# Performance work log

Measured on AMD Instinct MI355X. Metric: run time of the kernel, lower is better.

The kernel has to match this reference:

```python
import jax, jax.numpy as jnp
import numpy as np

IMG_DIM = 28 * 28


def _distmat(X):
    # D[i,j] = ||x_i||^2 - 2 x_i.x_j + ||x_j||^2
    r = jnp.sum(X * X, axis=1)
    a = X @ X.T
    return r[:, None] - 2.0 * a + r[None, :]


def _sigma_from_self(D, m):
    """Replicates sigma_estimation(X, X): median of the strict lower triangle of
    distmat(cat([X, X])), which is the 2x2 block-tiled matrix [[D,D],[D,D]].
    Its strict lower triangle multiset = full D (block 2,1) + 2x strict tril(D).
    Clamps: if med<=0 use mean; floor at 0.01. Detached (stop_gradient), matching
    the torch .detach().cpu().numpy() path."""
    mask = jnp.tril(jnp.ones((m, m), dtype=bool), -1)
    tril_inf = jnp.where(mask, D, jnp.inf)
    vals = jnp.concatenate([D.ravel(), tril_inf.ravel(), tril_inf.ravel()])
    s = jnp.sort(vals)  # inf padding sorts to the end
    k = 2 * m * m - m  # number of strict-lower-triangle entries of a 2m x 2m matrix
    if k % 2 == 0:
        med = 0.5 * (s[k // 2 - 1] + s[k // 2])  # np.median averages middles
    else:
        med = s[(k - 1) // 2]
    tri_sum = jnp.sum(jnp.where(mask, D, 0.0))
    mean_tri = (jnp.sum(D) + 2.0 * tri_sum) / k
    med = jnp.where(med <= 0.0, mean_tri, med)
    med = jnp.maximum(med, 0.01)
    return jax.lax.stop_gradient(med)


def _centered_kernel(D, sigma):
    # Kxc = Kx @ (I - ones/m)  ==  Kx - rowmean(Kx)
    K = jnp.exp(-D / (2.0 * sigma * sigma))
    return K - jnp.mean(K, axis=1, keepdims=True)


def _hsic_norm_from_kernels(Kxc, Kyc):
    Pxy = jnp.mean(Kxc * Kyc.T)
    Px = jnp.sqrt(jnp.mean(Kxc * Kxc.T))
    Py = jnp.sqrt(jnp.mean(Kyc * Kyc.T))
    return Pxy / (Px * Py)


def reference(x, y):
    x2 = x.reshape((-1, IMG_DIM))  # [m, 784]
    m = x2.shape[0]
    d = y.shape[-1]

    # hsic_normalized(x, y) with per-variable median sigma
    Dx = _distmat(x2)
    Dy = _distmat(y)
    Kx = _centered_kernel(Dx, _sigma_from_self(Dx, m))
    Ky = _centered_kernel(Dy, _sigma_from_self(Dy, m))
    mi_io = _hsic_norm_from_kernels(Kx, Ky)

    # Batched version of the nested loop over latent component pairs (i<j).
    # Per-column 1-D distance matrices: [d, m, m]
    yt = y.T  # [d, m]
    Dc = (yt[:, :, None] - yt[:, None, :]) ** 2
    sig = jax.vmap(lambda D: _sigma_from_self(D, m))(Dc)  # [d]
    Kc = jnp.exp(-Dc / (2.0 * sig * sig)[:, None, None])
    Kc = Kc - jnp.mean(Kc, axis=2, keepdims=True)  # centered, [d, m, m]

    # P[a,b] = mean(K_a * K_b^T)
    P = jnp.einsum('aij,bji->ab', Kc, Kc) / (m * m)
    diag = jnp.diagonal(P)
    norm = P / jnp.sqrt(diag[:, None] * diag[None, :])
    pair_mask = jnp.triu(jnp.ones((d, d), dtype=bool), 1)  # i < j
    mi_component_sum = jnp.sum(jnp.where(pair_mask, norm, 0.0))

    return -mi_io + mi_component_sum


def setup_inputs() -> dict:
    key = jax.random.key(0)
    kx, ky = jax.random.split(key)
    x = jax.random.normal(kx, (2048, 784), dtype=jnp.float32)
    y = jax.random.normal(ky, (2048, 10), dtype=jnp.float32)
    return {"x": x, "y": y}
```

## Files before the change

### kernel.cpp

```cpp
#include <hip/hip_runtime.h>
#include <math.h>

constexpr int Md   = 2048;
constexpr int NDIM = 784;
constexpr int DYC  = 10;
constexpr int MM   = Md * Md;
constexpr unsigned RANK_LO = 4193279u;
constexpr unsigned RANK_HI = 4193280u;
constexpr int NPROB = 12;
constexpr int NB    = 256;
constexpr int NBINS = 8192;
constexpr int NTRI  = 528;

constexpr size_t OFF_DX     = 0;
constexpr size_t OFF_DY     = OFF_DX + (size_t)MM * 4;
constexpr size_t OFF_RX     = OFF_DY + (size_t)MM * 4;
constexpr size_t OFF_RY     = OFF_RX + Md * 8;
constexpr size_t OFF_RC     = OFF_RY + Md * 8;
constexpr size_t OFF_GACC   = OFF_RC + (size_t)DYC * Md * 8;
constexpr size_t OFF_HISTA  = OFF_GACC + 64 * 8;
constexpr size_t OFF_HISTB  = OFF_HISTA + (size_t)NPROB * NBINS * 4;
constexpr size_t OFF_RES    = OFF_HISTB + (size_t)NPROB * NBINS * 4;
constexpr size_t OFF_JOBS   = OFF_RES + 72 * 8;
constexpr size_t OFF_Q      = OFF_JOBS + NPROB * 5 * 4;
constexpr size_t OFF_RXN    = OFF_Q + NPROB * 4;
constexpr size_t OFF_YT     = OFF_RXN + Md * 4;
constexpr size_t WS_NEED    = OFF_YT + (size_t)DYC * Md * 4;
constexpr size_t ZERO_BASE  = OFF_GACC;
constexpr size_t ZERO_LEN   = OFF_JOBS - OFF_GACC;

typedef _Float16 f16x8 __attribute__((ext_vector_type(8)));
typedef _Float16 f16x4 __attribute__((ext_vector_type(4)));
typedef float    f32x16 __attribute__((ext_vector_type(16)));

__device__ __forceinline__ unsigned fkey(float v) {
  unsigned u = __float_as_uint(v);
  return (u & 0x80000000u) ? ~u : (u | 0x80000000u);
}
__device__ __forceinline__ float keyinv(unsigned k) {
  unsigned u = (k & 0x80000000u) ? (k ^ 0x80000000u) : ~k;
  return __uint_as_float(u);
}
__device__ __forceinline__ f16x8 ld8(const _Float16* p) {
  f16x4 lo = *(const f16x4*)p;
  f16x4 hi = *(const f16x4*)(p + 4);
  f16x8 r;
  r[0]=lo[0]; r[1]=lo[1]; r[2]=lo[2]; r[3]=lo[3];
  r[4]=hi[0]; r[5]=hi[1]; r[6]=hi[2]; r[7]=hi[3];
  return r;
}
__device__ __forceinline__ double waveReduceD(double v) {
  #pragma unroll
  for (int o = 32; o > 0; o >>= 1) v += __shfl_down(v, o, 64);
  return v;
}
__device__ __forceinline__ double blockReduceD(double v) {
  __shared__ double sred[4];
  v = waveReduceD(v);
  int lane = threadIdx.x & 63;
  int w    = threadIdx.x >> 6;
  __syncthreads();
  if (lane == 0) sred[w] = v;
  __syncthreads();
  double r = 0.0;
  if (threadIdx.x == 0) { r = sred[0] + sred[1] + sred[2] + sred[3]; }
  return r;
}

__global__ void fail_kernel(float* out) { if (threadIdx.x == 0) out[0] = 0.0f; }

__global__ __launch_bounds__(256) void prep_kernel(const float* __restrict__ X,
                                                   const float* __restrict__ Y,
                                                   float* __restrict__ rxn,
                                                   float* __restrict__ Yt,
                                                   unsigned* __restrict__ jobs) {
  int bb = blockIdx.x;
  if (bb < Md) {
    double acc = 0.0;
    for (int k = threadIdx.x; k < NDIM; k += 256) {
      float v = X[bb * NDIM + k];
      acc += (double)v * (double)v;
    }
    double r = blockReduceD(acc);
    if (threadIdx.x == 0) rxn[bb] = (float)r;
  } else if (bb < Md + 80) {
    int e = (bb - Md) * 256 + threadIdx.x;
    if (e < Md * DYC) {
      int i = e / DYC, c = e % DYC;
      Yt[c * Md + i] = Y[e];
    }
  } else {
    int t = threadIdx.x;
    if (t < NPROB * 5) {
      int w = t % 5;
      jobs[t] = (w == 1) ? RANK_LO : (w == 3) ? RANK_HI : 0u;
    }
  }
}

__global__ __launch_bounds__(256) void dist_kernel(const float* __restrict__ X,
                                                   const float* __restrict__ Y,
                                                   const float* __restrict__ rxn,
                                                   float* __restrict__ Dx,
                                                   float* __restrict__ Dy) {
  __shared__ _Float16 Ah[64][68], Al[64][68], Bh[64][68], Bl[64][68];
  __shared__ float Yi[64][10], Yj[64][10];
  const int tid = threadIdx.x;
  int t0 = blockIdx.x;
  int bi = (int)((sqrtf(8.0f * (float)t0 + 1.0f) - 1.0f) * 0.5f);
  while ((bi + 1) * (bi + 2) / 2 <= t0) ++bi;
  while (bi * (bi + 1) / 2 > t0) --bi;
  int bj = t0 - bi * (bi + 1) / 2;
  const int i0 = bi * 64, j0 = bj * 64;
  const bool offdiag = (bi != bj);

  if (blockIdx.z == 1) {
    for (int t = tid; t < 640; t += 256) {
      int r = t / 10, c = t % 10;
      Yi[r][c] = Y[(i0 + r) * DYC + c];
      Yj[r][c] = Y[(j0 + r) * DYC + c];
    }
    __syncthreads();
    int jj = tid & 63;
    int ii0 = (tid >> 6) * 16;
    float yj[10];
    #pragma unroll
    for (int c = 0; c < 10; ++c) yj[c] = Yj[jj][c];
    for (int r = 0; r < 16; ++r) {
      int ii = ii0 + r;
      float s = 0.f;
      #pragma unroll
      for (int c = 0; c < 10; ++c) { float d = Yi[ii][c] - yj[c]; s = fmaf(d, d, s); }
      Dy[(size_t)(i0 + ii) * Md + (j0 + jj)] = s;
      if (offdiag) Dy[(size_t)(j0 + jj) * Md + (i0 + ii)] = s;
    }
    return;
  }

  const int wave = tid >> 6, lane = tid & 63;
  const int wr = (wave >> 1) * 32, wc = (wave & 1) * 32;
  const int srow = tid >> 2;
  const int sseg = (tid & 3) * 8;

  f32x16 acc_hh = {}, acc_c1 = {}, acc_c2 = {};

  const float* Arow = X + (size_t)(i0 + srow) * NDIM;
  const float* Brow = X + (size_t)(j0 + srow) * NDIM;
  const int lrow = lane & 31;
  const int lko  = (lane >> 5) * 8;

  for (int k0 = 0; k0 < 800; k0 += 32) {
    float a[8], b[8];
    if (k0 + 32 <= NDIM) {
      float4 a4 = *(const float4*)(Arow + k0 + sseg);
      float4 a5 = *(const float4*)(Arow + k0 + sseg + 4);
      float4 b4 = *(const float4*)(Brow + k0 + sseg);
      float4 b5 = *(const float4*)(Brow + k0 + sseg + 4);
      a[0]=a4.x; a[1]=a4.y; a[2]=a4.z; a[3]=a4.w; a[4]=a5.x; a[5]=a5.y; a[6]=a5.z; a[7]=a5.w;
      b[0]=b4.x; b[1]=b4.y; b[2]=b4.z; b[3]=b4.w; b[4]=b5.x; b[5]=b5.y; b[6]=b5.z; b[7]=b5.w;
    } else {
      #pragma unroll
      for (int u = 0; u < 8; ++u) {
        int k = k0 + sseg + u;
        a[u] = (k < NDIM) ? Arow[k] : 0.0f;
        b[u] = (k < NDIM) ? Brow[k] : 0.0f;
      }
    }
    __syncthreads();
    #pragma unroll
    for (int half = 0; half < 2; ++half) {
      f16x4 vah, val_, vbh, vbl;
      #pragma unroll
      for (int u = 0; u < 4; ++u) {
        float av = a[half * 4 + u];
        _Float16 h = (_Float16)av;
        vah[u] = h; val_[u] = (_Float16)(av - (float)h);
        float bv = b[half * 4 + u];
        _Float16 g = (_Float16)bv;
        vbh[u] = g; vbl[u] = (_Float16)(bv - (float)g);
      }
      *(f16x4*)&Ah[srow][sseg + half * 4] = vah;
      *(f16x4*)&Al[srow][sseg + half * 4] = val_;
      *(f16x4*)&Bh[srow][sseg + half * 4] = vbh;
      *(f16x4*)&Bl[srow][sseg + half * 4] = vbl;
    }
    __syncthreads();
    #pragma unroll
    for (int ks = 0; ks < 2; ++ks) {
      int ko = ks * 16 + lko;
      f16x8 fah = ld8(&Ah[wr + lrow][ko]);
      f16x8 fal = ld8(&Al[wr + lrow][ko]);
      f16x8 fbh = ld8(&Bh[wc + lrow][ko]);
      f16x8 fbl = ld8(&Bl[wc + lrow][ko]);
      acc_hh = __builtin_amdgcn_mfma_f32_32x32x16_f16(fah, fbh, acc_hh, 0, 0, 0);
      acc_c1 = __builtin_amdgcn_mfma_f32_32x32x16_f16(fah, fbl, acc_c1, 0, 0, 0);
      acc_c2 = __builtin_amdgcn_mfma_f32_32x32x16_f16(fal, fbh, acc_c2, 0, 0, 0);
    }
  }
  int col = j0 + wc + (lane & 31);
  float rj = rxn[col];
  #pragma unroll
  for (int r = 0; r < 16; ++r) {
    int row = i0 + wr + (r & 3) + 8 * (r >> 2) + 4 * (lane >> 5);
    float t = rxn[row] + rj;
    float cc = acc_c1[r] + acc_c2[r];
    float v = fmaf(-2.0f, cc, fmaf(-2.0f, acc_hh[r], t));
    Dx[(size_t)row * Md + col] = v;
    if (offdiag) Dx[(size_t)col * Md + row] = v;
  }
}

__global__ __launch_bounds__(256) void hist_kernel(const float* __restrict__ Dx,
                                                   const float* __restrict__ Dy,
                                                   const float* __restrict__ Yt,
                                                   unsigned* __restrict__ histA,
                                                   unsigned* __restrict__ histB,
                                                   const unsigned* __restrict__ jobs,
                                                   int level) {
  __shared__ unsigned lh[NBINS];
  __shared__ float ycol[Md];
  int prob = blockIdx.y;
  for (int b = threadIdx.x; b < NBINS; b += 256) lh[b] = 0;
  const float* Mptr = (prob == 0) ? Dx : (prob == 1 ? Dy : nullptr);
  if (prob >= 2) {
    const float* src = Yt + (size_t)(prob - 2) * Md;
    for (int i = threadIdx.x; i < Md; i += 256) ycol[i] = src[i];
  }
  __syncthreads();
  unsigned pfxL = jobs[prob * 5 + 0];
  unsigned pfxH = jobs[prob * 5 + 2];
  unsigned div  = jobs[prob * 5 + 4];
  unsigned* ghB = histB + prob * NBINS;

  auto histo = [&](float v, unsigned w) {
    unsigned key = fkey(v);
    if (level == 0) {
      atomicAdd(&lh[key >> 19], w);
    } else if (level == 1) {
      if ((key >> 19) == pfxL)             atomicAdd(&lh[(key >> 6) & 8191u], w);
      else if (div && (key >> 19) == pfxH) atomicAdd(&ghB[(key >> 6) & 8191u], w);
    } else {
      if ((key >> 6) == pfxL)              atomicAdd(&lh[key & 63u], w);
      else if (div && (key >> 6) == pfxH)  atomicAdd(&ghB[key & 63u], w);
    }
  };

  for (int r = 0; r < Md / NB; ++r) {
    int i = blockIdx.x + r * NB;
    int n = i + 1, ng = n >> 2, tail = n & 3;
    if (Mptr) {
      const float4* row4 = (const float4*)(Mptr + (size_t)i * Md);
      for (int g = threadIdx.x; g < ng; g += 256) {
        float4 v = row4[g];
        int jb = g << 2;
        histo(v.x, (jb == i) ? 1u : 4u);
        histo(v.y, (jb + 1 == i) ? 1u : 4u);
        histo(v.z, (jb + 2 == i) ? 1u : 4u);
        histo(v.w, (jb + 3 == i) ? 1u : 4u);
      }
      if (threadIdx.x < tail) {
        int j = (ng << 2) + threadIdx.x;
        histo(Mptr[(size_t)i * Md + j], (j == i) ? 1u : 4u);
      }
    } else {
      float yi = ycol[i];
      for (int g = threadIdx.x; g < ng; g += 256) {
        float4 y4 = *(const float4*)&ycol[g << 2];
        int jb = g << 2;
        float d0 = yi - y4.x, d1 = yi - y4.y, d2 = yi - y4.z, d3 = yi - y4.w;
        histo(d0 * d0, (jb == i) ? 1u : 4u);
        histo(d1 * d1, (jb + 1 == i) ? 1u : 4u);
        histo(d2 * d2, (jb + 2 == i) ? 1u : 4u);
        histo(d3 * d3, (jb + 3 == i) ? 1u : 4u);
      }
      if (threadIdx.x < tail) {
        int j = (ng << 2) + threadIdx.x;
        float d = yi - ycol[j];
        histo(d * d, (j == i) ? 1u : 4u);
      }
    }
  }
  __syncthreads();
  unsigned* ghA = histA + prob * NBINS;
  for (int b = threadIdx.x; b < NBINS; b += 256) {
    unsigned v = lh[b];
    if (v) atomicAdd(&ghA[b], v);
  }
}

__global__ __launch_bounds__(256) void select_kernel(unsigned* __restrict__ histA,
                                                     unsigned* __restrict__ histB,
                                                     unsigned* __restrict__ jobs,
                                                     float* __restrict__ q,
                                                     int level) {
  __shared__ unsigned lhA[NBINS], lhB[NBINS];
  __shared__ unsigned psA[256], psB[256];
  int prob = blockIdx.x;
  int nbins = (level == 2) ? 64 : NBINS;
  int C = (nbins + 255) / 256;
  unsigned* ghA = histA + prob * NBINS;
  unsigned* ghB = histB + prob * NBINS;
  unsigned sA = 0, sB = 0;
  for (int k = 0; k < C; ++k) {
    int b = threadIdx.x * C + k;
    if (b < nbins) {
      unsigned v = ghA[b]; lhA[b] = v; sA += v;
      unsigned u = ghB[b]; lhB[b] = u; sB += u;
    }
  }
  psA[threadIdx.x] = sA; psB[threadIdx.x] = sB;
  __syncthreads();
  if (threadIdx.x == 0) {
    unsigned pfxL = jobs[prob * 5 + 0], remL = jobs[prob * 5 + 1];
    unsigned pfxH = jobs[prob * 5 + 2], remH = jobs[prob * 5 + 3];
    unsigned wasdiv = jobs[prob * 5 + 4];

    auto scan = [&](const unsigned* ps, const unsigned* lhp, unsigned r,
                    int& bin, unsigned& cum) {
      unsigned c = 0; int t = 0;
      for (; t < 255; ++t) { if (c + ps[t] > r) break; c += ps[t]; }
      int b = t * C;
      int be = b + C - 1; if (be > nbins - 1) be = nbins - 1;
      for (; b < be; ++b) { if (c + lhp[b] > r) break; c += lhp[b]; }
      bin = b; cum = c;
    };

    int bL; unsigned cL; scan(psA, lhA, remL, bL, cL);
    int bH; unsigned cH;
    unsigned div = wasdiv;
    if (!wasdiv) {
      scan(psA, lhA, remH, bH, cH);
      if (bH != bL) div = 1;
    } else {
      scan(psB, lhB, remH, bH, cH);
    }
    unsigned baseH = wasdiv ? pfxH : pfxL;
    if (level < 2) {
      jobs[prob * 5 + 0] = (level == 0) ? (unsigned)bL : ((pfxL << 13) | (unsigned)bL);
      jobs[prob * 5 + 2] = (level == 0) ? (unsigned)bH : ((baseH << 13) | (unsigned)bH);
      jobs[prob * 5 + 1] = remL - cL;
      jobs[prob * 5 + 3] = remH - cH;
      jobs[prob * 5 + 4] = div;
    } else {
      unsigned keyL = (pfxL << 6) | (unsigned)bL;
      unsigned keyH = (baseH << 6) | (unsigned)bH;
      float med = 0.5f * (keyinv(keyL) + keyinv(keyH));
      med = fmaxf(med, 0.01f);
      q[prob] = 2.0f * med * med;
    }
  }
  __syncthreads();
  for (int b = threadIdx.x; b < nbins; b += 256) { ghA[b] = 0; ghB[b] = 0; }
}

__global__ __launch_bounds__(256) void phase3a_kernel(const float* __restrict__ Dx,
                                                      const float* __restrict__ Dy,
                                                      const float* __restrict__ Yt,
                                                      const float* __restrict__ q,
                                                      double* __restrict__ Rx,
                                                      double* __restrict__ Ry,
                                                      double* __restrict__ Rc,
                                                      double* __restrict__ gacc) {
  __shared__ double shred[12];
  const int wave = threadIdx.x >> 6, lane = threadIdx.x & 63;
  int bb = blockIdx.x;

  if (bb < 256) {
    const float qx = q[0], qy = q[1];
    double gxx = 0, gxy = 0, gyy = 0;
    #pragma unroll
    for (int rr = 0; rr < 2; ++rr) {
      int i = bb * 4 + wave + rr * 1024;
      const float4* rx4 = (const float4*)(Dx + (size_t)i * Md);
      const float4* ry4 = (const float4*)(Dy + (size_t)i * Md);
      double ax = 0, ay = 0;
      #pragma unroll
      for (int it = 0; it < 8; ++it) {
        float4 xv = rx4[it * 64 + lane];
        float4 yv = ry4[it * 64 + lane];
        #pragma unroll
        for (int u = 0; u < 4; ++u) {
          float xe = (u == 0) ? xv.x : (u == 1) ? xv.y : (u == 2) ? xv.z : xv.w;
          float ye = (u == 0) ? yv.x : (u == 1) ? yv.y : (u == 2) ? yv.z : yv.w;
          float ex = expm1f(-(xe / qx));
          float ey = expm1f(-(ye / qy));
          ax += (double)ex; ay += (double)ey;
          gxx += (double)ex * ex;
          gxy += (double)ex * ey;
          gyy += (double)ey * ey;
        }
      }
      ax = waveReduceD(ax);
      ay = waveReduceD(ay);
      if (lane == 0) { Rx[i] = ax; Ry[i] = ay; }
    }
    gxx = waveReduceD(gxx);
    gxy = waveReduceD(gxy);
    gyy = waveReduceD(gyy);
    if (lane == 0) { shred[wave] = gxx; shred[4 + wave] = gxy; shred[8 + wave] = gyy; }
    __syncthreads();
    if (threadIdx.x == 0) {
      atomicAdd(&gacc[0], shred[0] + shred[1] + shred[2] + shred[3]);
      atomicAdd(&gacc[1], shred[4] + shred[5] + shred[6] + shred[7]);
      atomicAdd(&gacc[2], shred[8] + shred[9] + shred[10] + shred[11]);
    }
  } else {
    int i = (bb - 256) * 4 + wave;
    float yi[10], ninv[10];
    #pragma unroll
    for (int c = 0; c < 10; ++c) { yi[c] = Yt[c * Md + i]; ninv[c] = -1.0f / q[2 + c]; }
    float facc[10] = {};
    #pragma unroll 2
    for (int it = 0; it < 8; ++it) {
      int j = it * 256 + lane * 4;
      #pragma unroll
      for (int c = 0; c < 10; ++c) {
        float4 v = *(const float4*)(Yt + c * Md + j);
        float d0 = yi[c] - v.x, d1 = yi[c] - v.y, d2 = yi[c] - v.z, d3 = yi[c] - v.w;
        facc[c] += __expf(d0 * d0 * ninv[c]) - 1.0f;
        facc[c] += __expf(d1 * d1 * ninv[c]) - 1.0f;
        facc[c] += __expf(d2 * d2 * ninv[c]) - 1.0f;
        facc[c] += __expf(d3 * d3 * ninv[c]) - 1.0f;
      }
    }
    #pragma unroll
    for (int c = 0; c < 10; ++c) {
      double r = waveReduceD((double)facc[c]);
      if (lane == 0) Rc[c * Md + i] = r;
    }
  }
}

__global__ __launch_bounds__(256) void comp_grand_kernel(const float* __restrict__ Yt,
                                                         const float* __restrict__ q,
                                                         double* __restrict__ gacc) {
  __shared__ double shred[220];
  const int wave = threadIdx.x >> 6, lane = threadIdx.x & 63;
  float ninv[10];
  #pragma unroll
  for (int c = 0; c < 10; ++c) ninv[c] = -1.0f / q[2 + c];
  int tid0 = blockIdx.x * 256 + threadIdx.x;
  int j = tid0 & 2047;
  float yj[10];
  #pragma unroll
  for (int c = 0; c < 10; ++c) yj[c] = Yt[c * Md + j];
  float facc[55];
  #pragma unroll
  for (int k = 0; k < 55; ++k) facc[k] = 0.0f;
  for (int i = tid0 >> 11; i < Md; i += 64) {
    float e[10];
    #pragma unroll
    for (int c = 0; c < 10; ++c) {
      float d = Yt[c * Md + i] - yj[c];
      e[c] = __expf(d * d * ninv[c]) - 1.0f;
    }
    int k = 0;
    #pragma unroll
    for (int a = 0; a < 10; ++a)
      #pragma unroll
      for (int b = a; b < 10; ++b) { facc[k] = fmaf(e[a], e[b], facc[k]); ++k; }
  }
  #pragma unroll
  for (int k = 0; k < 55; ++k) {
    double v = waveReduceD((double)facc[k]);
    if (lane == 0) shred[k * 4 + wave] = v;
  }
  __syncthreads();
  for (int k = threadIdx.x; k < 55; k += 256) {
    double v = shred[k * 4] + shred[k * 4 + 1] + shred[k * 4 + 2] + shred[k * 4 + 3];
    atomicAdd(&gacc[3 + k], v);
  }
}

__global__ __launch_bounds__(256) void final_sums_kernel(const double* __restrict__ Rx,
                                                         const double* __restrict__ Ry,
                                                         const double* __restrict__ Rc,
                                                         double* __restrict__ res) {
  int k = blockIdx.x;
  double acc = 0.0;
  if (k < 5) {
    for (int i = threadIdx.x; i < Md; i += 256) {
      double a = Rx[i], b = Ry[i];
      acc += (k == 0) ? a : (k == 1) ? b : (k == 2) ? a * b : (k == 3) ? a * a : b * b;
    }
  } else if (k < 15) {
    const double* p = Rc + (size_t)(k - 5) * Md;
    for (int i = threadIdx.x; i < Md; i += 256) acc += p[i];
  } else {
    int kk = k - 15;
    int a = 0;
    while (kk >= 10 - a) { kk -= 10 - a; ++a; }
    int b = a + kk;
    const double* pa = Rc + (size_t)a * Md;
    const double* pb = Rc + (size_t)b * Md;
    for (int i = threadIdx.x; i < Md; i += 256) acc += pa[i] * pb[i];
  }
  double r = blockReduceD(acc);
  if (threadIdx.x == 0) res[k] = r;
}

__global__ void final_combine_kernel(const double* __restrict__ res,
                                     const double* __restrict__ gacc,
                                     float* __restrict__ out) {
  if (threadIdx.x != 0) return;
  const double m = (double)Md, m2 = m * m;
  double Gxx = gacc[0], Gxy = gacc[1], Gyy = gacc[2];
  double Sxy = Gxy - (2.0 / m) * res[2] + (res[0] * res[1]) / m2;
  double Sxx = Gxx - (2.0 / m) * res[3] + (res[0] * res[0]) / m2;
  double Syy = Gyy - (2.0 / m) * res[4] + (res[1] * res[1]) / m2;
  double mi_io = Sxy / sqrt(Sxx * Syy);

  double Sc[55], diag[10];
  int k = 0;
  for (int a = 0; a < 10; ++a)
    for (int b = a; b < 10; ++b) {
      double S = gacc[3 + k] - (2.0 / m) * res[15 + k] + (res[5 + a] * res[5 + b]) / m2;
      Sc[k] = S;
      if (a == b) diag[a] = S;
      ++k;
    }
  double comp = 0.0;
  k = 0;
  for (int a = 0; a < 10; ++a)
    for (int b = a; b < 10; ++b) {
      if (b > a) comp += Sc[k] / sqrt(diag[a] * diag[b]);
      ++k;
    }
  out[0] = (float)(-mi_io + comp);
}

extern "C" void kernel_launch(void* const* d_in, const int* in_sizes, int n_in,
                              void* d_out, int out_size, void* d_ws, size_t ws_size,
                              hipStream_t stream) {
  const float* X = (const float*)d_in[0];
  const float* Y = (const float*)d_in[1];
  float* out = (float*)d_out;
  char* ws = (char*)d_ws;

  if (ws_size < WS_NEED) {
    fail_kernel<<<1, 64, 0, stream>>>(out);
    return;
  }

  float*    Dx    = (float*)(ws + OFF_DX);
  float*    Dy    = (float*)(ws + OFF_DY);
  double*   Rx    = (double*)(ws + OFF_RX);
  double*   Ry    = (double*)(ws + OFF_RY);
  double*   Rc    = (double*)(ws + OFF_RC);
  double*   gacc  = (double*)(ws + OFF_GACC);
  unsigned* histA = (unsigned*)(ws + OFF_HISTA);
  unsigned* histB = (unsigned*)(ws + OFF_HISTB);
  double*   res   = (double*)(ws + OFF_RES);
  unsigned* jobs  = (unsigned*)(ws + OFF_JOBS);
  float*    q     = (float*)(ws + OFF_Q);
  float*    rxn   = (float*)(ws + OFF_RXN);
  float*    Yt    = (float*)(ws + OFF_YT);

  hipMemsetAsync(ws + ZERO_BASE, 0, ZERO_LEN, stream);
  prep_kernel<<<Md + 80 + 1, 256, 0, stream>>>(X, Y, rxn, Yt, jobs);
  dist_kernel<<<dim3(NTRI, 1, 2), 256, 0, stream>>>(X, Y, rxn, Dx, Dy);

  for (int lvl = 0; lvl < 3; ++lvl) {
    hist_kernel<<<dim3(NB, NPROB), 256, 0, stream>>>(Dx, Dy, Yt, histA, histB, jobs, lvl);
    select_kernel<<<NPROB, 256, 0, stream>>>(histA, histB, jobs, q, lvl);
  }

  phase3a_kernel<<<768, 256, 0, stream>>>(Dx, Dy, Yt, q, Rx, Ry, Rc, gacc);
  comp_grand_kernel<<<512, 256, 0, stream>>>(Yt, q, gacc);
  final_sums_kernel<<<70, 256, 0, stream>>>(Rx, Ry, Rc, res);
  final_combine_kernel<<<1, 64, 0, stream>>>(res, gacc, out);
}
```

Before: 428.5 us.

## Histogram full symmetric matrix with weight 2 instead of triangular rows

The median-selection histogram pass now walks the whole distance matrix in flat, perfectly coalesced float4 chunks with weight 2. It subtracts the diagonal with a wrapping negative weight, in place of walking only the lower triangle row by row with per-element weights of 1 or 4. This removes the load imbalance and divergence of triangular rows and the per-element diagonal checks, at the cost of reading about twice as many elements. For the y-columns it assumes a zero diagonal and applies a single correction. Local histogram clearing and flushing are also limited to 64 bins at the last level.

```diff
diff --git a/kernel.cpp b/kernel.cpp
--- a/kernel.cpp
+++ b/kernel.cpp
@@ -220,7 +220,8 @@
   __shared__ unsigned lh[NBINS];
   __shared__ float ycol[Md];
   int prob = blockIdx.y;
-  for (int b = threadIdx.x; b < NBINS; b += 256) lh[b] = 0;
+  int nbins = (level == 2) ? 64 : NBINS;
+  for (int b = threadIdx.x; b < nbins; b += 256) lh[b] = 0;
   const float* Mptr = (prob == 0) ? Dx : (prob == 1 ? Dy : nullptr);
   if (prob >= 2) {
     const float* src = Yt + (size_t)(prob - 2) * Md;
@@ -245,44 +246,42 @@
     }
   };
 
-  for (int r = 0; r < Md / NB; ++r) {
-    int i = blockIdx.x + r * NB;
-    int n = i + 1, ng = n >> 2, tail = n & 3;
-    if (Mptr) {
-      const float4* row4 = (const float4*)(Mptr + (size_t)i * Md);
-      for (int g = threadIdx.x; g < ng; g += 256) {
-        float4 v = row4[g];
-        int jb = g << 2;
-        histo(v.x, (jb == i) ? 1u : 4u);
-        histo(v.y, (jb + 1 == i) ? 1u : 4u);
-        histo(v.z, (jb + 2 == i) ? 1u : 4u);
-        histo(v.w, (jb + 3 == i) ? 1u : 4u);
+  if (Mptr) {
+    const float4* M4 = (const float4*)Mptr + (size_t)blockIdx.x * 4096;
+    #pragma unroll 1
+    for (int it = 0; it < 16; it += 4) {
+      float4 v0 = M4[(it + 0) * 256 + threadIdx.x];
+      float4 v1 = M4[(it + 1) * 256 + threadIdx.x];
+      float4 v2 = M4[(it + 2) * 256 + threadIdx.x];
+      float4 v3 = M4[(it + 3) * 256 + threadIdx.x];
+      histo(v0.x, 2u); histo(v0.y, 2u); histo(v0.z, 2u); histo(v0.w, 2u);
+      histo(v1.x, 2u); histo(v1.y, 2u); histo(v1.z, 2u); histo(v1.w, 2u);
+      histo(v2.x, 2u); histo(v2.y, 2u); histo(v2.z, 2u); histo(v2.w, 2u);
+      histo(v3.x, 2u); histo(v3.y, 2u); histo(v3.z, 2u); histo(v3.w, 2u);
+    }
+    if (prob == 0 && blockIdx.x == 0) {
+      for (int i = threadIdx.x; i < Md; i += 256)
+        histo(Mptr[(size_t)i * Md + i], 0xFFFFFFFFu);
+    }
+  } else {
+    int row0 = blockIdx.x * 8;
+    #pragma unroll 1
+    for (int r = 0; r < 8; ++r) {
+      float yi = ycol[row0 + r];
+      #pragma unroll
+      for (int g = 0; g < 2; ++g) {
+        float4 y4 = *(const float4*)&ycol[(g * 256 + threadIdx.x) * 4];
+        float d0 = yi - y4.x, d1 = yi - y4.y, d2 = yi - y4.z, d3 = yi - y4.w;
+        histo(d0 * d0, 2u); histo(d1 * d1, 2u);
+        histo(d2 * d2, 2u); histo(d3 * d3, 2u);
       }
-      if (threadIdx.x < tail) {
-        int j = (ng << 2) + threadIdx.x;
-        histo(Mptr[(size_t)i * Md + j], (j == i) ? 1u : 4u);
-      }
-    } else {
-      float yi = ycol[i];
-      for (int g = threadIdx.x; g < ng; g += 256) {
-        float4 y4 = *(const float4*)&ycol[g << 2];
-        int jb = g << 2;
-        float d0 = yi - y4.x, d1 = yi - y4.y, d2 = yi - y4.z, d3 = yi - y4.w;
-        histo(d0 * d0, (jb == i) ? 1u : 4u);
-        histo(d1 * d1, (jb + 1 == i) ? 1u : 4u);
-        histo(d2 * d2, (jb + 2 == i) ? 1u : 4u);
-        histo(d3 * d3, (jb + 3 == i) ? 1u : 4u);
-      }
-      if (threadIdx.x < tail) {
-        int j = (ng << 2) + threadIdx.x;
-        float d = yi - ycol[j];
-        histo(d * d, (j == i) ? 1u : 4u);
-      }
-    }
+    }
+    if (blockIdx.x == 0 && threadIdx.x == 0)
+      histo(0.0f, (unsigned)(-(int)Md));
   }
   __syncthreads();
   unsigned* ghA = histA + prob * NBINS;
-  for (int b = threadIdx.x; b < NBINS; b += 256) {
+  for (int b = threadIdx.x; b < nbins; b += 256) {
     unsigned v = lh[b];
     if (v) atomicAdd(&ghA[b], v);
   }
```

Measured after the change: 436.9 us. Within noise of the previous version (+2.0%).
